# Performance work log

Hardware: AMD Instinct MI355X
Metric: run time of the kernel (lower is better)

Reference implementation:

```python
import jax, jax.numpy as jnp
import numpy as np

B, CQ, CKV, H, W = 8, 192, 192, 128, 128
NUM_HEADS = 6
KERNEL_SIZES = (7, 9, 11)
K_BRANCHES = 3
H_I = NUM_HEADS // K_BRANCHES          # heads per branch = 2
DIM_PROJ = 192
HEAD_DIM = DIM_PROJ // NUM_HEADS       # 32
BRANCH_CH = DIM_PROJ // K_BRANCHES     # 64 channels per branch (H_I * HEAD_DIM)
SCALE = HEAD_DIM ** -0.5


def _na2d_branch(q, k, v, ksize, rpb):
    """Neighborhood attention 2D, dilation=1, clamped window (NATTEN semantics).
    q,k,v: [B, h, H, W, d]; rpb: [h, 2K-1, 2K-1] or None. Returns [B, h, H, W, d]."""
    Bq, h, Hq, Wq, d = q.shape
    K = ksize
    NS = K // 2
    # window start clamped so every query sees exactly K keys per axis
    rows = jnp.clip(jnp.arange(Hq) - NS, 0, Hq - K)[:, None] + jnp.arange(K)  # [H, K]
    cols = jnp.clip(jnp.arange(Wq) - NS, 0, Wq - K)[:, None] + jnp.arange(K)  # [W, K]
    qs = q * SCALE
    # scores: loop over the K row-taps (small fixed kernel), vectorized over everything else
    attn_rows = []
    for ki in range(K):
        kr = k[:, :, rows[:, ki]]          # [B,h,H,W,d]  gather key rows
        kc = kr[:, :, :, cols]             # [B,h,H,W,K,d] gather key cols
        attn_rows.append(jnp.einsum('bhijd,bhijkd->bhijk', qs, kc))
    attn = jnp.stack(attn_rows, axis=4)    # [B,h,H,W,K,K]
    if rpb is not None:
        # bias index = (key_pos - query_pos) + (K-1) on each axis
        rel_r = rows - jnp.arange(Hq)[:, None] + (K - 1)   # [H,K] in [0, 2K-2]
        rel_c = cols - jnp.arange(Wq)[:, None] + (K - 1)   # [W,K]
        bias = rpb[:, rel_r][:, :, :, rel_c]               # [h,H,K,W,K]
        bias = jnp.transpose(bias, (0, 1, 3, 2, 4))        # [h,H,W,K,K]
        attn = attn + bias[None]
    attn = jax.nn.softmax(attn.reshape(Bq, h, Hq, Wq, K * K), axis=-1)
    attn = attn.reshape(Bq, h, Hq, Wq, K, K)
    out = jnp.zeros((Bq, h, Hq, Wq, d), q.dtype)
    for ki in range(K):
        vr = v[:, :, rows[:, ki]]          # [B,h,H,W,d]
        vc = vr[:, :, :, cols]             # [B,h,H,W,K,d]
        out = out + jnp.einsum('bhijk,bhijkd->bhijd', attn[:, :, :, :, ki], vc)
    return out


def setup_inputs() -> dict:
    key = jax.random.key(0)
    ks = jax.random.split(key, 16)
    inp = {
        'x': jax.random.normal(ks[0], (B, CQ, H, W), jnp.float32),
        'context': jax.random.normal(ks[1], (B, CKV, H, W), jnp.float32),
        'Wq': jax.random.normal(ks[2], (CQ, DIM_PROJ), jnp.float32) * 0.02,
        'bq': jax.random.normal(ks[3], (DIM_PROJ,), jnp.float32) * 0.02,
        'Wk': jax.random.normal(ks[4], (CKV, DIM_PROJ), jnp.float32) * 0.02,
        'bk': jax.random.normal(ks[5], (DIM_PROJ,), jnp.float32) * 0.02,
        'Wv': jax.random.normal(ks[6], (CKV, DIM_PROJ), jnp.float32) * 0.02,
        'bv': jax.random.normal(ks[7], (DIM_PROJ,), jnp.float32) * 0.02,
        'Wo': jax.random.normal(ks[8], (DIM_PROJ, CQ), jnp.float32) * 0.02,
        'bo': jax.random.normal(ks[9], (CQ,), jnp.float32) * 0.02,
        'rpb0': jax.random.normal(ks[10], (H_I, 2 * 7 - 1, 2 * 7 - 1), jnp.float32) * 0.02,
        'rpb1': jax.random.normal(ks[11], (H_I, 2 * 9 - 1, 2 * 9 - 1), jnp.float32) * 0.02,
        'rpb2': jax.random.normal(ks[12], (H_I, 2 * 11 - 1, 2 * 11 - 1), jnp.float32) * 0.02,
    }
    return inp


def reference(x, context, Wq, bq, Wk, bk, Wv, bv, Wo, bo, rpb0, rpb1, rpb2):
    rpbs = (rpb0, rpb1, rpb2)
    xc = jnp.transpose(x, (0, 2, 3, 1))        # [B,H,W,Cq]
    ctx = jnp.transpose(context, (0, 2, 3, 1))  # [B,H,W,Ckv]
    q = xc @ Wq + bq                            # [B,H,W,192]
    k = ctx @ Wk + bk
    v = ctx @ Wv + bv
    outs = []
    for i, ksize in enumerate(KERNEL_SIZES):
        sl = slice(i * BRANCH_CH, (i + 1) * BRANCH_CH)
        def to_heads(t):
            return jnp.transpose(
                t[..., sl].reshape(B, H, W, H_I, HEAD_DIM), (0, 3, 1, 2, 4))
        o = _na2d_branch(to_heads(q), to_heads(k), to_heads(v), ksize, rpbs[i])
        outs.append(jnp.transpose(o, (0, 2, 3, 1, 4)).reshape(B, H, W, BRANCH_CH))
    out = jnp.concatenate(outs, axis=-1) @ Wo + bo   # [B,H,W,Cq]
    return jnp.transpose(out, (0, 3, 1, 2))          # [B,Cq,H,W]
```

## Files before the change

### kernel.cpp

```cpp
#include <hip/hip_runtime.h>
#include <hip/hip_fp16.h>

#define HH 128
#define WW 128
#define NPIX (HH*WW)
#define NB 8
#define NHEADS 6
#define HD 32
#define SCALE 0.17677669529663687f
#define LOG2E 1.4426950408889634f
#define QSCALE (SCALE * LOG2E)

typedef _Float16 h2 __attribute__((ext_vector_type(2)));
typedef __fp16 g2 __attribute__((ext_vector_type(2)));
typedef _Float16 f16x4 __attribute__((ext_vector_type(4)));
typedef _Float16 f16x8 __attribute__((ext_vector_type(8)));
typedef float f4 __attribute__((ext_vector_type(4)));
typedef float f2 __attribute__((ext_vector_type(2)));

#if __has_builtin(__builtin_amdgcn_exp2f)
#define EXP2(x) __builtin_amdgcn_exp2f(x)
#else
#define EXP2(x) exp2f(x)
#endif

#define LDK 40
union U4 { g2 p2[2]; f16x4 v4; };

__global__ __launch_bounds__(512) void prep_wt(
    const float* __restrict__ Wq, const float* __restrict__ Wk,
    const float* __restrict__ Wv, _Float16* __restrict__ wt)
{
    int idx = blockIdx.x * 512 + threadIdx.x;
    int mat = idx / 36864, rem = idx % 36864;
    int k = rem / 192, n = rem % 192;
    const float* W = mat == 0 ? Wq : (mat == 1 ? Wk : Wv);
    wt[(size_t)mat * 36864 + (size_t)n * 192 + k] = (_Float16)W[(size_t)k * 192 + n];
}

__global__ __launch_bounds__(512) void prep_wo(
    const float* __restrict__ Wo, _Float16* __restrict__ woT)
{
    int idx = blockIdx.x * 512 + threadIdx.x;
    int k = idx / 192, n = idx % 192;
    woT[(size_t)n * 192 + k] = (_Float16)Wo[(size_t)k * 192 + n];
}

__global__ __launch_bounds__(512, 4) void proj_mfma(
    const float* __restrict__ x, const float* __restrict__ ctx,
    const _Float16* __restrict__ wt,
    const float* __restrict__ bq, const float* __restrict__ bk, const float* __restrict__ bv,
    _Float16* __restrict__ qh, _Float16* __restrict__ kh, _Float16* __restrict__ vh)
{
    int bid = blockIdx.x;
    int xcd = bid & 7;
    int i = bid >> 3;
    bool is_q = (i < 128);
    int xb = xcd * 128 + (is_q ? i : i - 128);

    const float* A = is_q ? x : ctx;

    __shared__ _Float16 Ts[128 * 192];

    int t = threadIdx.x;
    int m0 = xb * 128;
    int b  = m0 / NPIX;
    int p0 = m0 % NPIX;
    const float* Ab = A + (size_t)b * 192 * NPIX + p0;

    int lane = t & 63;
    int wid  = t >> 6;
    int wm = wid & 1;
    int wn = wid >> 1;
    int lq = lane & 15;
    int lk = lane >> 4;

    {
        int pq = t & 31;
        int cg = t >> 5;
        int c_base = cg * 12;
        f4 ra[12];
        #pragma unroll
        for (int j = 0; j < 12; j++)
            ra[j] = __builtin_nontemporal_load((const f4*)&Ab[(size_t)(c_base + j) * NPIX + 4 * pq]);
        __builtin_amdgcn_sched_barrier(0);
        #pragma unroll
        for (int r = 0; r < 4; r++) {
            int pix = 4 * pq + r;
            int sw = (pix & 7) << 3;
            #pragma unroll
            for (int j4 = 0; j4 < 3; j4++) {
                int c0 = c_base + j4 * 4;
                U4 u;
                u.p2[0] = __builtin_amdgcn_cvt_pkrtz(ra[j4 * 4][r],     ra[j4 * 4 + 1][r]);
                u.p2[1] = __builtin_amdgcn_cvt_pkrtz(ra[j4 * 4 + 2][r], ra[j4 * 4 + 3][r]);
                *(f16x4*)&Ts[pix * 192 + (c0 ^ sw)] = u.v4;
            }
        }
    }
    __syncthreads();

    if (is_q) {
        const _Float16* WT = wt;
        f4 acc[12] = {};
        #pragma unroll
        for (int ks = 0; ks < 6; ks++) {
            f16x8 wf[3];
            #pragma unroll
            for (int ni = 0; ni < 3; ni++)
                wf[ni] = *(const f16x8*)&WT[(size_t)(wn * 48 + ni * 16 + lq) * 192 + ks * 32 + lk * 8];
            #pragma unroll
            for (int mi = 0; mi < 4; mi++) {
                int pix = wm * 64 + mi * 16 + lq;
                f16x8 pfr = *(const f16x8*)&Ts[pix * 192 + ((ks * 32 + lk * 8) ^ ((pix & 7) << 3))];
                __builtin_amdgcn_s_setprio(1);
                #pragma unroll
                for (int ni = 0; ni < 3; ni++)
                    acc[mi * 3 + ni] = __builtin_amdgcn_mfma_f32_16x16x32_f16(wf[ni], pfr, acc[mi * 3 + ni], 0, 0, 0);
                __builtin_amdgcn_s_setprio(0);
            }
        }
        __syncthreads();

        #pragma unroll
        for (int mi = 0; mi < 4; mi++) {
            int pix = wm * 64 + mi * 16 + lq;
            int sw = (pix & 7) << 3;
            #pragma unroll
            for (int ni = 0; ni < 3; ni++) {
                int n0 = wn * 48 + ni * 16 + lk * 4;
                f4 v = acc[mi * 3 + ni];
                f4 bb = *(const f4*)&bq[n0];
                U4 u;
                u.p2[0] = __builtin_amdgcn_cvt_pkrtz((v[0] + bb[0]) * QSCALE, (v[1] + bb[1]) * QSCALE);
                u.p2[1] = __builtin_amdgcn_cvt_pkrtz((v[2] + bb[2]) * QSCALE, (v[3] + bb[3]) * QSCALE);
                *(f16x4*)&Ts[pix * 192 + (n0 ^ sw)] = u.v4;
            }
        }
        __syncthreads();

        int p2 = t >> 2, qc = t & 3;
        int sw = (p2 & 7) << 3;
        #pragma unroll
        for (int g = 0; g < 6; g++) {
            f16x8 val = *(const f16x8*)&Ts[p2 * 192 + ((g * 32 + qc * 8) ^ sw)];
            *(f16x8*)(qh + ((size_t)(b * NHEADS + g) * NPIX + p0 + p2) * HD + qc * 8) = val;
        }
    } else {
        #pragma unroll
        for (int out = 0; out < 2; out++) {
            const _Float16* WT = wt + (size_t)(1 + out) * 36864;
            const float* bias = out == 0 ? bk : bv;
            _Float16* outp = out == 0 ? kh : vh;
            f4 acc[12] = {};
            #pragma unroll
            for (int ks = 0; ks < 6; ks++) {
                f16x8 wf[3];
                #pragma unroll
                for (int ni = 0; ni < 3; ni++)
                    wf[ni] = *(const f16x8*)&WT[(size_t)(wn * 48 + ni * 16 + lq) * 192 + ks * 32 + lk * 8];
                #pragma unroll
                for (int mi = 0; mi < 4; mi++) {
                    int pix = wm * 64 + mi * 16 + lq;
                    f16x8 pfr = *(const f16x8*)&Ts[pix * 192 + ((ks * 32 + lk * 8) ^ ((pix & 7) << 3))];
                    __builtin_amdgcn_s_setprio(1);
                    #pragma unroll
                    for (int ni = 0; ni < 3; ni++)
                        acc[mi * 3 + ni] = __builtin_amdgcn_mfma_f32_16x16x32_f16(wf[ni], pfr, acc[mi * 3 + ni], 0, 0, 0);
                    __builtin_amdgcn_s_setprio(0);
                }
            }
            #pragma unroll
            for (int mi = 0; mi < 4; mi++) {
                int p = p0 + wm * 64 + mi * 16 + lq;
                #pragma unroll
                for (int ni = 0; ni < 3; ni++) {
                    int n0 = wn * 48 + ni * 16 + lk * 4;
                    int g = n0 >> 5, d0 = n0 & 31;
                    f4 v = acc[mi * 3 + ni];
                    f4 bb = *(const f4*)&bias[n0];
                    U4 u;
                    u.p2[0] = __builtin_amdgcn_cvt_pkrtz(v[0] + bb[0], v[1] + bb[1]);
                    u.p2[1] = __builtin_amdgcn_cvt_pkrtz(v[2] + bb[2], v[3] + bb[3]);
                    *(f16x4*)(outp + ((size_t)(b * NHEADS + g) * NPIX + p) * HD + d0) = u.v4;
                }
            }
        }
    }
}

#define NA2D_SMEM 68352

template<int K>
__device__ __forceinline__ void na2d_tile(
    const _Float16* __restrict__ qh, const _Float16* __restrict__ kh,
    const _Float16* __restrict__ vh, const float* __restrict__ rpb,
    _Float16* __restrict__ ah, char* smem, int b, int g_head, int hi, int ty, int tx)
{
    constexpr int NS = K / 2;
    constexpr int RW = 2 * K - 1;
    _Float16* Vt = (_Float16*)smem;
    float* rpbs = (float*)(smem + 66560);

    int t = threadIdx.x;
    size_t plane = (size_t)(b * NHEADS + g_head) * NPIX;
    int h0 = ty * 16, w0 = tx * 16;
    int rmin = min(max(h0 - NS, 0), HH - K);
    int rtop = min(max(h0 + 15 - NS, 0), HH - K);
    int rows_n = rtop + K - rmin;
    int cwin0 = min(max(w0 - NS, 0), WW - K);
    int ctop = min(max(w0 + 15 - NS, 0), WW - K);
    int cols_n = ctop + K - cwin0;

    for (int i = t; i < RW * RW; i += 512) rpbs[i] = rpb[(size_t)hi * RW * RW + i] * LOG2E;

    int ntask = rows_n * 128;
    for (int idx = t; idx < ntask; idx += 512) {
        int row = idx >> 7;
        int key = (idx >> 2) & 31;
        int dc  = idx & 3;
        f16x8 vvv = {0,0,0,0,0,0,0,0};
        if (key < cols_n) {
            size_t pix = plane + (size_t)(rmin + row) * WW + (cwin0 + key);
            vvv = *(const f16x8*)&vh[pix * HD + dc * 8];
        }
        int m = 8 * ((key & 15) >> 2) + 4 * (key >> 4) + (key & 3);
        #pragma unroll
        for (int j = 0; j < 8; j++)
            Vt[row * 1280 + (dc * 8 + j) * LDK + m] = vvv[j];
    }
    __syncthreads();

    int lane = t & 63, wid = t >> 6;
    int lq = lane & 15, lg = lane >> 4;
    int wq = w0 + lq;
    int c0q = min(max(wq - NS, 0), WW - K);
    int klo = c0q - cwin0;
    int shiftc = cwin0 - wq + K - 1;
    f4 zf4 = {0.f, 0.f, 0.f, 0.f};

    int rcx[2][4];
    bool vld[2][4];
    #pragma unroll
    for (int c = 0; c < 2; c++) {
        #pragma unroll
        for (int r = 0; r < 4; r++) {
            int key_local = c * 16 + 4 * lg + r;
            rcx[c][r] = min(max(key_local + shiftc, 0), RW - 1);
            vld[c][r] = (unsigned)(key_local - klo) < (unsigned)K;
        }
    }
    h2 one2 = {(_Float16)1.f, (_Float16)1.f};

    #pragma unroll 1
    for (int qi = 0; qi < 2; qi++) {
        int qr = wid * 2 + qi;
        int h = h0 + qr;
        int r0q = min(max(h - NS, 0), HH - K);
        int row_base = r0q - rmin;
        f16x8 qf = *(const f16x8*)&qh[(plane + (size_t)h * WW + w0 + lq) * HD + lg * 8];
        f4 acc0 = zf4, acc1 = zf4;
        float lsum = 0.f;

        #pragma unroll 1
        for (int ki = 0; ki < K; ki++) {
            int row = row_base + ki;
            const _Float16* kgrow = kh + (plane + (size_t)(rmin + row) * WW + cwin0) * HD;
            f16x8 a0 = *(const f16x8*)&kgrow[(size_t)lq * HD + lg * 8];
            f16x8 a1 = *(const f16x8*)&kgrow[(size_t)(16 + lq) * HD + lg * 8];
            __builtin_amdgcn_s_setprio(1);
            f4 s0 = __builtin_amdgcn_mfma_f32_16x16x32_f16(a0, qf, zf4, 0, 0, 0);
            f4 s1 = __builtin_amdgcn_mfma_f32_16x16x32_f16(a1, qf, zf4, 0, 0, 0);
            __builtin_amdgcn_s_setprio(0);

            int rel_r = r0q + ki - h + K - 1;
            const float* rrow = rpbs + rel_r * RW;
            float pf[2][4];
            #pragma unroll
            for (int c = 0; c < 2; c++) {
                #pragma unroll
                for (int r = 0; r < 4; r++) {
                    float sv = (c ? s1[r] : s0[r]) + rrow[rcx[c][r]];
                    pf[c][r] = vld[c][r] ? EXP2(sv) : 0.f;
                }
            }
            union { g2 p[4]; h2 ph[4]; f16x8 v; } P;
            P.p[0] = __builtin_amdgcn_cvt_pkrtz(pf[0][0], pf[0][1]);
            P.p[1] = __builtin_amdgcn_cvt_pkrtz(pf[0][2], pf[0][3]);
            P.p[2] = __builtin_amdgcn_cvt_pkrtz(pf[1][0], pf[1][1]);
            P.p[3] = __builtin_amdgcn_cvt_pkrtz(pf[1][2], pf[1][3]);
            lsum = __builtin_amdgcn_fdot2(P.ph[0], one2, lsum, false);
            lsum = __builtin_amdgcn_fdot2(P.ph[1], one2, lsum, false);
            lsum = __builtin_amdgcn_fdot2(P.ph[2], one2, lsum, false);
            lsum = __builtin_amdgcn_fdot2(P.ph[3], one2, lsum, false);

            const _Float16* vbase = &Vt[row * 1280 + lg * 8];
            f16x8 b0 = *(const f16x8*)&vbase[lq * LDK];
            f16x8 b1 = *(const f16x8*)&vbase[(16 + lq) * LDK];
            __builtin_amdgcn_s_setprio(1);
            acc0 = __builtin_amdgcn_mfma_f32_16x16x32_f16(P.v, b0, acc0, 0, 0, 0);
            acc1 = __builtin_amdgcn_mfma_f32_16x16x32_f16(P.v, b1, acc1, 0, 0, 0);
            __builtin_amdgcn_s_setprio(0);
        }

        lsum += __shfl_xor(lsum, 16);
        lsum += __shfl_xor(lsum, 32);
        float inv = 1.f / lsum;
        _Float16* obase = ah + (plane + (size_t)h * WW + w0) * HD;
        #pragma unroll
        for (int r = 0; r < 4; r++) {
            float ir = __shfl(inv, 4 * lg + r);
            obase[(4 * lg + r) * HD + lq]      = (_Float16)(acc0[r] * ir);
            obase[(4 * lg + r) * HD + lq + 16] = (_Float16)(acc1[r] * ir);
        }
    }
}

__global__ __launch_bounds__(512) void na2d_mfma(
    const _Float16* __restrict__ qh, const _Float16* __restrict__ kh,
    const _Float16* __restrict__ vh,
    const float* __restrict__ rpb0, const float* __restrict__ rpb1,
    const float* __restrict__ rpb2, _Float16* __restrict__ ah)
{
    extern __shared__ char smem[];
    int bid = blockIdx.x;
    int xcd = bid & 7;
    int i = bid >> 3;
    int phase = i >> 7;
    int j = i & 127;
    int lb = xcd * 128 + j;
    int bz = lb >> 6;
    int tile = lb & 63;
    int b = bz >> 1, hi = bz & 1;
    int ty = tile >> 3, tx = tile & 7;
    if (phase == 0)      na2d_tile<7>(qh, kh, vh, rpb0, ah, smem, b, 0 + hi, hi, ty, tx);
    else if (phase == 1) na2d_tile<9>(qh, kh, vh, rpb1, ah, smem, b, 2 + hi, hi, ty, tx);
    else                 na2d_tile<11>(qh, kh, vh, rpb2, ah, smem, b, 4 + hi, hi, ty, tx);
}

__global__ __launch_bounds__(512) void oproj_mfma(
    const _Float16* __restrict__ ah, const _Float16* __restrict__ woT,
    const float* __restrict__ bo, float* __restrict__ outp)
{
    int t = threadIdx.x;
    int m0 = blockIdx.x * 128;
    int b  = m0 / NPIX;
    int p0 = m0 % NPIX;

    int lane = t & 63;
    int wid  = t >> 6;
    int wm = wid & 1;
    int wn = wid >> 1;
    int lr = lane & 15;
    int lk = lane >> 4;

    f4 acc[4][3] = {};

    #pragma unroll
    for (int ks = 0; ks < 6; ks++) {
        const _Float16* abase = ah + (size_t)(b * NHEADS + ks) * NPIX * HD;
        f16x8 af[4], bf[3];
        #pragma unroll
        for (int mi = 0; mi < 4; mi++)
            af[mi] = *(const f16x8*)&abase[(size_t)(p0 + wm * 64 + mi * 16 + lr) * HD + lk * 8];
        #pragma unroll
        for (int ni = 0; ni < 3; ni++)
            bf[ni] = *(const f16x8*)&woT[(size_t)(wn * 48 + ni * 16 + lr) * 192 + ks * 32 + lk * 8];
        #pragma unroll
        for (int mi = 0; mi < 4; mi++)
            #pragma unroll
            for (int ni = 0; ni < 3; ni++)
                acc[mi][ni] = __builtin_amdgcn_mfma_f32_16x16x32_f16(af[mi], bf[ni], acc[mi][ni], 0, 0, 0);
    }

    #pragma unroll
    for (int ni = 0; ni < 3; ni++) {
        int n = wn * 48 + ni * 16 + lr;
        float bb = bo[n];
        float* obase = outp + ((size_t)b * 192 + n) * NPIX + p0 + wm * 64;
        #pragma unroll
        for (int mi = 0; mi < 4; mi++) {
            f4 v = acc[mi][ni];
            v[0] += bb; v[1] += bb; v[2] += bb; v[3] += bb;
            *(f4*)&obase[mi * 16 + lk * 4] = v;
        }
    }
}

extern "C" void kernel_launch(void* const* d_in, const int* in_sizes, int n_in,
                              void* d_out, int out_size, void* d_ws, size_t ws_size,
                              hipStream_t stream) {
    const float* x    = (const float*)d_in[0];
    const float* ctx  = (const float*)d_in[1];
    const float* Wq   = (const float*)d_in[2];
    const float* bq   = (const float*)d_in[3];
    const float* Wk   = (const float*)d_in[4];
    const float* bk   = (const float*)d_in[5];
    const float* Wv   = (const float*)d_in[6];
    const float* bv   = (const float*)d_in[7];
    const float* Wo   = (const float*)d_in[8];
    const float* bo   = (const float*)d_in[9];
    const float* rpb0 = (const float*)d_in[10];
    const float* rpb1 = (const float*)d_in[11];
    const float* rpb2 = (const float*)d_in[12];

    size_t N = (size_t)NB * NHEADS * NPIX * HD;
    _Float16* qh = (_Float16*)d_ws;
    _Float16* kh = qh + N;
    _Float16* vh = kh + N;
    _Float16* ah = vh + N;
    float* outp = (float*)d_out;

    _Float16* wt  = (_Float16*)d_out + N;
    _Float16* woT = qh;

    (void)hipFuncSetAttribute((const void*)na2d_mfma,
                              hipFuncAttributeMaxDynamicSharedMemorySize, NA2D_SMEM);

    prep_wt<<<216, 512, 0, stream>>>(Wq, Wk, Wv, wt);
    proj_mfma<<<2048, 512, 0, stream>>>(x, ctx, wt, bq, bk, bv, qh, kh, vh);
    na2d_mfma<<<3072, 512, NA2D_SMEM, stream>>>(qh, kh, vh, rpb0, rpb1, rpb2, ah);
    prep_wo<<<72, 512, 0, stream>>>(Wo, woT);
    oproj_mfma<<<1024, 512, 0, stream>>>(ah, woT, bo, outp);
}
```

Before: 235.9 us.

## Rebalance projection blocks into 64-pixel KV tiles and fold RPB into MFMA accumulator

The projection kernel splits K/V work into 64-pixel tiles, so each block does roughly the same MFMA work as a 128-pixel Q block. It also interleaves Q and KV blocks (phase = i%3) and launches 3072 blocks instead of 2048. This is meant to reduce tail imbalance, since KV blocks previously did twice the work of Q blocks. In the neighborhood-attention kernel the relative position bias is loaded before the QK MFMA and passed in as the accumulator init, which removes the separate add after the MFMA and lets the bias loads overlap the K fetch. The smaller KV tiles reload weight fragments more often per pixel and use a more irregular LDS store pattern.

Result: slower. 265.3 us (+12.5%).

```diff
diff --git a/kernel.cpp b/kernel.cpp
--- a/kernel.cpp
+++ b/kernel.cpp
@@ -16,7 +16,6 @@
 typedef _Float16 f16x4 __attribute__((ext_vector_type(4)));
 typedef _Float16 f16x8 __attribute__((ext_vector_type(8)));
 typedef float f4 __attribute__((ext_vector_type(4)));
-typedef float f2 __attribute__((ext_vector_type(2)));
 
 #if __has_builtin(__builtin_amdgcn_exp2f)
 #define EXP2(x) __builtin_amdgcn_exp2f(x)
@@ -55,52 +54,51 @@
     int bid = blockIdx.x;
     int xcd = bid & 7;
     int i = bid >> 3;
-    bool is_q = (i < 128);
-    int xb = xcd * 128 + (is_q ? i : i - 128);
-
-    const float* A = is_q ? x : ctx;
+    int phase = i % 3;
+    int base = i / 3;
+    bool is_q = (phase == 0);
 
     __shared__ _Float16 Ts[128 * 192];
 
     int t = threadIdx.x;
-    int m0 = xb * 128;
-    int b  = m0 / NPIX;
-    int p0 = m0 % NPIX;
-    const float* Ab = A + (size_t)b * 192 * NPIX + p0;
-
     int lane = t & 63;
     int wid  = t >> 6;
-    int wm = wid & 1;
-    int wn = wid >> 1;
     int lq = lane & 15;
     int lk = lane >> 4;
 
-    {
-        int pq = t & 31;
-        int cg = t >> 5;
-        int c_base = cg * 12;
-        f4 ra[12];
-        #pragma unroll
-        for (int j = 0; j < 12; j++)
-            ra[j] = __builtin_nontemporal_load((const f4*)&Ab[(size_t)(c_base + j) * NPIX + 4 * pq]);
-        __builtin_amdgcn_sched_barrier(0);
-        #pragma unroll
-        for (int r = 0; r < 4; r++) {
-            int pix = 4 * pq + r;
-            int sw = (pix & 7) << 3;
-            #pragma unroll
-            for (int j4 = 0; j4 < 3; j4++) {
-                int c0 = c_base + j4 * 4;
-                U4 u;
-                u.p2[0] = __builtin_amdgcn_cvt_pkrtz(ra[j4 * 4][r],     ra[j4 * 4 + 1][r]);
-                u.p2[1] = __builtin_amdgcn_cvt_pkrtz(ra[j4 * 4 + 2][r], ra[j4 * 4 + 3][r]);
-                *(f16x4*)&Ts[pix * 192 + (c0 ^ sw)] = u.v4;
-            }
-        }
-    }
-    __syncthreads();
-
     if (is_q) {
+        int m0 = (xcd * 128 + base) * 128;
+        int b  = m0 / NPIX;
+        int p0 = m0 % NPIX;
+        const float* Ab = x + (size_t)b * 192 * NPIX + p0;
+        int wm = wid & 1;
+        int wn = wid >> 1;
+
+        {
+            int pq = t & 31;
+            int cg = t >> 5;
+            int c_base = cg * 12;
+            f4 ra[12];
+            #pragma unroll
+            for (int j = 0; j < 12; j++)
+                ra[j] = __builtin_nontemporal_load((const f4*)&Ab[(size_t)(c_base + j) * NPIX + 4 * pq]);
+            __builtin_amdgcn_sched_barrier(0);
+            #pragma unroll
+            for (int r = 0; r < 4; r++) {
+                int pix = 4 * pq + r;
+                int sw = (pix & 7) << 3;
+                #pragma unroll
+                for (int j4 = 0; j4 < 3; j4++) {
+                    int c0 = c_base + j4 * 4;
+                    U4 u;
+                    u.p2[0] = __builtin_amdgcn_cvt_pkrtz(ra[j4 * 4][r],     ra[j4 * 4 + 1][r]);
+                    u.p2[1] = __builtin_amdgcn_cvt_pkrtz(ra[j4 * 4 + 2][r], ra[j4 * 4 + 3][r]);
+                    *(f16x4*)&Ts[pix * 192 + (c0 ^ sw)] = u.v4;
+                }
+            }
+        }
+        __syncthreads();
+
         const _Float16* WT = wt;
         f4 acc[12] = {};
         #pragma unroll
@@ -147,12 +145,50 @@
             *(f16x8*)(qh + ((size_t)(b * NHEADS + g) * NPIX + p0 + p2) * HD + qc * 8) = val;
         }
     } else {
+        int tile = xcd * 256 + 2 * base + (phase - 1);
+        int m0 = tile * 64;
+        int b  = m0 / NPIX;
+        int p0 = m0 % NPIX;
+        const float* Ab = ctx + (size_t)b * 192 * NPIX + p0;
+        int wm = wid & 1;
+        int wn = wid >> 1;
+
+        {
+            int pq = t & 15;
+            int cg = t >> 4;
+            int c_base = cg * 6;
+            f4 ra[6];
+            #pragma unroll
+            for (int j = 0; j < 6; j++)
+                ra[j] = __builtin_nontemporal_load((const f4*)&Ab[(size_t)(c_base + j) * NPIX + 4 * pq]);
+            __builtin_amdgcn_sched_barrier(0);
+            #pragma unroll
+            for (int r = 0; r < 4; r++) {
+                int pix = 4 * pq + r;
+                int sw = (pix & 7) << 3;
+                U4 u;
+                u.p2[0] = __builtin_amdgcn_cvt_pkrtz(ra[0][r], ra[1][r]);
+                u.p2[1] = __builtin_amdgcn_cvt_pkrtz(ra[2][r], ra[3][r]);
+                if ((c_base & 3) == 0) {
+                    *(f16x4*)&Ts[pix * 192 + (c_base ^ sw)] = u.v4;
+                    *(g2*)&Ts[pix * 192 + ((c_base + 4) ^ sw)] = __builtin_amdgcn_cvt_pkrtz(ra[4][r], ra[5][r]);
+                } else {
+                    *(g2*)&Ts[pix * 192 + (c_base ^ sw)] = u.p2[0];
+                    U4 v2;
+                    v2.p2[0] = __builtin_amdgcn_cvt_pkrtz(ra[2][r], ra[3][r]);
+                    v2.p2[1] = __builtin_amdgcn_cvt_pkrtz(ra[4][r], ra[5][r]);
+                    *(f16x4*)&Ts[pix * 192 + ((c_base + 2) ^ sw)] = v2.v4;
+                }
+            }
+        }
+        __syncthreads();
+
         #pragma unroll
         for (int out = 0; out < 2; out++) {
             const _Float16* WT = wt + (size_t)(1 + out) * 36864;
             const float* bias = out == 0 ? bk : bv;
             _Float16* outp = out == 0 ? kh : vh;
-            f4 acc[12] = {};
+            f4 acc[6] = {};
             #pragma unroll
             for (int ks = 0; ks < 6; ks++) {
                 f16x8 wf[3];
@@ -160,8 +196,8 @@
                 for (int ni = 0; ni < 3; ni++)
                     wf[ni] = *(const f16x8*)&WT[(size_t)(wn * 48 + ni * 16 + lq) * 192 + ks * 32 + lk * 8];
                 #pragma unroll
-                for (int mi = 0; mi < 4; mi++) {
-                    int pix = wm * 64 + mi * 16 + lq;
+                for (int mi = 0; mi < 2; mi++) {
+                    int pix = wm * 32 + mi * 16 + lq;
                     f16x8 pfr = *(const f16x8*)&Ts[pix * 192 + ((ks * 32 + lk * 8) ^ ((pix & 7) << 3))];
                     __builtin_amdgcn_s_setprio(1);
                     #pragma unroll
@@ -171,8 +207,8 @@
                 }
             }
             #pragma unroll
-            for (int mi = 0; mi < 4; mi++) {
-                int p = p0 + wm * 64 + mi * 16 + lq;
+            for (int mi = 0; mi < 2; mi++) {
+                int p = p0 + wm * 32 + mi * 16 + lq;
                 #pragma unroll
                 for (int ni = 0; ni < 3; ni++) {
                     int n0 = wn * 48 + ni * 16 + lk * 4;
@@ -265,22 +301,26 @@
         #pragma unroll 1
         for (int ki = 0; ki < K; ki++) {
             int row = row_base + ki;
+            int rel_r = r0q + ki - h + K - 1;
+            const float* rrow = rpbs + rel_r * RW;
+            f4 cb0, cb1;
+            #pragma unroll
+            for (int r = 0; r < 4; r++) { cb0[r] = rrow[rcx[0][r]]; cb1[r] = rrow[rcx[1][r]]; }
+
             const _Float16* kgrow = kh + (plane + (size_t)(rmin + row) * WW + cwin0) * HD;
             f16x8 a0 = *(const f16x8*)&kgrow[(size_t)lq * HD + lg * 8];
             f16x8 a1 = *(const f16x8*)&kgrow[(size_t)(16 + lq) * HD + lg * 8];
             __builtin_amdgcn_s_setprio(1);
-            f4 s0 = __builtin_amdgcn_mfma_f32_16x16x32_f16(a0, qf, zf4, 0, 0, 0);
-            f4 s1 = __builtin_amdgcn_mfma_f32_16x16x32_f16(a1, qf, zf4, 0, 0, 0);
+            f4 s0 = __builtin_amdgcn_mfma_f32_16x16x32_f16(a0, qf, cb0, 0, 0, 0);
+            f4 s1 = __builtin_amdgcn_mfma_f32_16x16x32_f16(a1, qf, cb1, 0, 0, 0);
             __builtin_amdgcn_s_setprio(0);
 
-            int rel_r = r0q + ki - h + K - 1;
-            const float* rrow = rpbs + rel_r * RW;
             float pf[2][4];
             #pragma unroll
             for (int c = 0; c < 2; c++) {
                 #pragma unroll
                 for (int r = 0; r < 4; r++) {
-                    float sv = (c ? s1[r] : s0[r]) + rrow[rcx[c][r]];
+                    float sv = c ? s1[r] : s0[r];
                     pf[c][r] = vld[c][r] ? EXP2(sv) : 0.f;
                 }
             }
@@ -418,7 +458,7 @@
                               hipFuncAttributeMaxDynamicSharedMemorySize, NA2D_SMEM);
 
     prep_wt<<<216, 512, 0, stream>>>(Wq, Wk, Wv, wt);
-    proj_mfma<<<2048, 512, 0, stream>>>(x, ctx, wt, bq, bk, bv, qh, kh, vh);
+    proj_mfma<<<3072, 512, 0, stream>>>(x, ctx, wt, bq, bk, bv, qh, kh, vh);
     na2d_mfma<<<3072, 512, NA2D_SMEM, stream>>>(qh, kh, vh, rpb0, rpb1, rpb2, ah);
     prep_wo<<<72, 512, 0, stream>>>(Wo, woT);
     oproj_mfma<<<1024, 512, 0, stream>>>(ah, woT, bo, outp);
```
